# Kernel tuning notes

Hardware: AMD Instinct MI355X
Metric: run time of the kernel (lower is better)

Reference implementation:

```python
import jax, jax.numpy as jnp
import numpy as np

EPS = 0.01  # added to std devs per the docstring to avoid div by zero


def _patches(A, p, H_out, W_out):
    # A: padded [B, D, Hp, Wp] -> [B, D, H_out, W_out, p*p] 5x5 neighborhoods
    return jnp.stack([A[:, :, u:u + H_out, v:v + W_out]
                      for u in range(p) for v in range(p)], axis=-1)


def _normalize(P):
    mu = P.mean(axis=-1, keepdims=True)
    sd = P.std(axis=-1, keepdims=True)  # population std over the p*p patch
    return (P - mu) / (sd + EPS)


def setup_inputs() -> dict:
    key = jax.random.key(0)
    k1, k2 = jax.random.split(key)
    B, D, H, W = 16, 64, 48, 24
    X = jax.random.normal(k1, (B, D, H, W), dtype=jnp.float32)
    Y = jax.random.normal(k2, (B, D, H, W), dtype=jnp.float32)
    return {"X": X, "Y": Y, "patch_size": 5}


def reference(X, Y, patch_size):
    B, D, H, W = X.shape
    p = patch_size
    d = p // 2
    n = p * p
    # X padded d on all sides; Y gets extra vertical padding (2*d) so patches
    # centered at rows x-d .. x+d are valid for every x.
    Xp = jnp.pad(X, ((0, 0), (0, 0), (d, d), (d, d)))
    Yp = jnp.pad(Y, ((0, 0), (0, 0), (2 * d, 2 * d), (d, d)))
    En = _normalize(_patches(Xp, p, H, W))             # [B,D,H,W,n]
    Fn = _normalize(_patches(Yp, p, H + 2 * d, W))     # [B,D,H+2d,W,n]
    # vertical search offsets a-d in [-d, d]: Fs[a] holds Y patches at row x+a-d
    Fs = jnp.stack([Fn[:, :, a:a + H] for a in range(2 * d + 1)], axis=0)  # [p,B,D,H,W,n]
    # ncc(E,F) = mean_k En_k * Fn_k ; output channel order: depth i, then
    # vertical offset a, then Y column c (out_depth = p * W * D)
    out = jnp.einsum('bdxyk,abdxck->bdacxy', En, Fs) / n  # [B,D,p,W,H,W]
    return out.reshape(B, D * p * W, H, W)
```

## Files before the change

### kernel.cpp

```cpp
#include <hip/hip_runtime.h>


#define BH 48
#define BW 24
constexpr float EPS = 0.01f;

__global__ __launch_bounds__(192, 3) void ncc_kernel(const float* __restrict__ X,
                                                     const float* __restrict__ Y,
                                                     float* __restrict__ out) {
    __shared__ float Xp[52 * 28];
    __shared__ float Yp[56 * 28];
    __shared__ float invYs[52 * 24];

    const int bd  = blockIdx.x;
    const int tid = threadIdx.x;

    const float* Xg = X + (size_t)bd * (BH * BW);
    const float* Yg = Y + (size_t)bd * (BH * BW);

    for (int i = tid; i < 52 * 28; i += 192) {
        int r = i / 28, c = i % 28;
        int orr = r - 2, oc = c - 2;
        float v = 0.f;
        if (orr >= 0 && orr < BH && oc >= 0 && oc < BW) v = Xg[orr * BW + oc];
        Xp[i] = v;
    }
    for (int i = tid; i < 56 * 28; i += 192) {
        int r = i / 28, c = i % 28;
        int orr = r - 4, oc = c - 2;
        float v = 0.f;
        if (orr >= 0 && orr < BH && oc >= 0 && oc < BW) v = Yg[orr * BW + oc];
        Yp[i] = v;
    }
    __syncthreads();

    for (int i = tid; i < 52 * 24; i += 192) {
        int r = i / 24, c = i % 24;
        float s = 0.f, s2 = 0.f;
#pragma unroll
        for (int u = 0; u < 5; ++u)
#pragma unroll
            for (int v = 0; v < 5; ++v) {
                float val = Yp[(r + u) * 28 + (c + v)];
                s += val;
                s2 += val * val;
            }
        float mu  = s * 0.04f;
        float var = fmaxf(s2 * 0.04f - mu * mu, 0.f);
        invYs[i] = 1.f / (sqrtf(var) + EPS);
    }
    __syncthreads();

    const int y  = tid % 24;
    const int xs = tid / 24;
    float* ob0 = out + (size_t)bd * (5 * 24 * 48 * 24);

    for (int xi = 0; xi < 6; ++xi) {
        const int x = xi * 8 + xs;

        float xn[25];
        float s = 0.f, s2 = 0.f;
#pragma unroll
        for (int u = 0; u < 5; ++u)
#pragma unroll
            for (int v = 0; v < 5; ++v) {
                float val = Xp[(x + u) * 28 + (y + v)];
                xn[u * 5 + v] = val;
                s += val;
                s2 += val * val;
            }
        float mu  = s * 0.04f;
        float var = fmaxf(s2 * 0.04f - mu * mu, 0.f);
        float inv = 1.f / (sqrtf(var) + EPS);
#pragma unroll
        for (int k = 0; k < 25; ++k) xn[k] = (xn[k] - mu) * inv;

        float* ob = ob0 + x * 24 + y;

        for (int a = 0; a < 5; ++a) {
            const int yr = x + a;

            float w[25];
#pragma unroll
            for (int u = 0; u < 5; ++u)
#pragma unroll
                for (int sc = 0; sc < 5; ++sc)
                    w[u * 5 + sc] = Yp[(yr + u) * 28 + sc];

#pragma unroll
            for (int c = 0; c < 24; ++c) {
                float dot = 0.f;
#pragma unroll
                for (int u = 0; u < 5; ++u)
#pragma unroll
                    for (int v = 0; v < 5; ++v)
                        dot += xn[u * 5 + v] * w[u * 5 + ((c + v) % 5)];
                ob[(size_t)(a * 24 + c) * (48 * 24)] =
                    dot * invYs[yr * 24 + c] * 0.04f;
                if (c < 23) {
#pragma unroll
                    for (int u = 0; u < 5; ++u)
                        w[u * 5 + (c % 5)] = Yp[(yr + u) * 28 + (c + 5)];
                }
            }
        }
    }
}

extern "C" void kernel_launch(void* const* d_in, const int* in_sizes, int n_in,
                              void* d_out, int out_size, void* d_ws, size_t ws_size,
                              hipStream_t stream) {
    const float* X = (const float*)d_in[0];
    const float* Y = (const float*)d_in[1];
    float* out = (float*)d_out;
    ncc_kernel<<<dim3(1024), dim3(192), 0, stream>>>(X, Y, out);
}
```

Measured before the change: 611.3 us.

## Share Y column window across vertical offsets with transposed padded shared layout

New measurement: 618.4 us. No clear change (+1.2%).

```diff
diff --git a/kernel.cpp b/kernel.cpp
--- a/kernel.cpp
+++ b/kernel.cpp
@@ -5,12 +5,16 @@
 #define BW 24
 constexpr float EPS = 0.01f;
 
+#define XPS 29
+#define YTS 57
+#define IVS 53
+
 __global__ __launch_bounds__(192, 3) void ncc_kernel(const float* __restrict__ X,
                                                      const float* __restrict__ Y,
                                                      float* __restrict__ out) {
-    __shared__ float Xp[52 * 28];
-    __shared__ float Yp[56 * 28];
-    __shared__ float invYs[52 * 24];
+    __shared__ float Xp[52 * XPS];
+    __shared__ float YpT[28 * YTS];
+    __shared__ float invYT[24 * IVS];
 
     const int bd  = blockIdx.x;
     const int tid = threadIdx.x;
@@ -23,31 +27,31 @@
         int orr = r - 2, oc = c - 2;
         float v = 0.f;
         if (orr >= 0 && orr < BH && oc >= 0 && oc < BW) v = Xg[orr * BW + oc];
-        Xp[i] = v;
+        Xp[r * XPS + c] = v;
     }
     for (int i = tid; i < 56 * 28; i += 192) {
         int r = i / 28, c = i % 28;
         int orr = r - 4, oc = c - 2;
         float v = 0.f;
         if (orr >= 0 && orr < BH && oc >= 0 && oc < BW) v = Yg[orr * BW + oc];
-        Yp[i] = v;
+        YpT[c * YTS + r] = v;
     }
     __syncthreads();
 
     for (int i = tid; i < 52 * 24; i += 192) {
-        int r = i / 24, c = i % 24;
+        int c = i % 24, r = i / 24;
         float s = 0.f, s2 = 0.f;
 #pragma unroll
-        for (int u = 0; u < 5; ++u)
+        for (int v = 0; v < 5; ++v)
 #pragma unroll
-            for (int v = 0; v < 5; ++v) {
-                float val = Yp[(r + u) * 28 + (c + v)];
+            for (int u = 0; u < 5; ++u) {
+                float val = YpT[(c + v) * YTS + (r + u)];
                 s += val;
                 s2 += val * val;
             }
         float mu  = s * 0.04f;
         float var = fmaxf(s2 * 0.04f - mu * mu, 0.f);
-        invYs[i] = 1.f / (sqrtf(var) + EPS);
+        invYT[c * IVS + r] = 1.f / (sqrtf(var) + EPS);
     }
     __syncthreads();
 
@@ -55,6 +59,7 @@
     const int xs = tid / 24;
     float* ob0 = out + (size_t)bd * (5 * 24 * 48 * 24);
 
+#pragma unroll 1
     for (int xi = 0; xi < 6; ++xi) {
         const int x = xi * 8 + xs;
 
@@ -64,44 +69,48 @@
         for (int u = 0; u < 5; ++u)
 #pragma unroll
             for (int v = 0; v < 5; ++v) {
-                float val = Xp[(x + u) * 28 + (y + v)];
+                float val = Xp[(x + u) * XPS + (y + v)];
                 xn[u * 5 + v] = val;
                 s += val;
                 s2 += val * val;
             }
         float mu  = s * 0.04f;
         float var = fmaxf(s2 * 0.04f - mu * mu, 0.f);
-        float inv = 1.f / (sqrtf(var) + EPS);
+        float sc  = 0.04f / (sqrtf(var) + EPS);
 #pragma unroll
-        for (int k = 0; k < 25; ++k) xn[k] = (xn[k] - mu) * inv;
+        for (int k = 0; k < 25; ++k) xn[k] = (xn[k] - mu) * sc;
 
         float* ob = ob0 + x * 24 + y;
 
-        for (int a = 0; a < 5; ++a) {
-            const int yr = x + a;
+        float w[5][9];
+#pragma unroll
+        for (int v = 0; v < 5; ++v)
+#pragma unroll
+            for (int r = 0; r < 9; ++r)
+                w[v][r] = YpT[v * YTS + x + r];
 
-            float w[25];
+#pragma unroll
+        for (int c = 0; c < 24; ++c) {
+            float dot[5] = {0.f, 0.f, 0.f, 0.f, 0.f};
 #pragma unroll
             for (int u = 0; u < 5; ++u)
 #pragma unroll
-                for (int sc = 0; sc < 5; ++sc)
-                    w[u * 5 + sc] = Yp[(yr + u) * 28 + sc];
-
+                for (int v = 0; v < 5; ++v) {
+                    const float f  = xn[u * 5 + v];
+                    const int  sl  = (c + v) % 5;
 #pragma unroll
-            for (int c = 0; c < 24; ++c) {
-                float dot = 0.f;
+                    for (int a = 0; a < 5; ++a)
+                        dot[a] += f * w[sl][a + u];
+                }
 #pragma unroll
-                for (int u = 0; u < 5; ++u)
+            for (int a = 0; a < 5; ++a) {
+                float iv = invYT[c * IVS + (x + a)];
+                ob[(size_t)(a * 24 + c) * (48 * 24)] = dot[a] * iv;
+            }
+            if (c < 23) {
 #pragma unroll
-                    for (int v = 0; v < 5; ++v)
-                        dot += xn[u * 5 + v] * w[u * 5 + ((c + v) % 5)];
-                ob[(size_t)(a * 24 + c) * (48 * 24)] =
-                    dot * invYs[yr * 24 + c] * 0.04f;
-                if (c < 23) {
-#pragma unroll
-                    for (int u = 0; u < 5; ++u)
-                        w[u * 5 + (c % 5)] = Yp[(yr + u) * 28 + (c + 5)];
-                }
+                for (int r = 0; r < 9; ++r)
+                    w[c % 5][r] = YpT[(c + 5) * YTS + x + r];
             }
         }
     }
```
